# Optimization experiments

Measured on AMD Instinct MI355X. Metric: run time of the kernel, lower is better.

Reference implementation:

```python
import jax, jax.numpy as jnp
import numpy as np

NUM_HEADS = 4
WORD_DIM = 100
LEAKY_ALPHA = 0.3  # keras LeakyReLU default negative_slope


def setup_inputs() -> dict:
    key = jax.random.key(0)
    k1, k2, k3 = jax.random.split(key, 3)
    x = jax.random.normal(k1, (8, 30, 20, 40, WORD_DIM), dtype=jnp.float32)
    # keras 'random_normal' initializer: stddev 0.05
    w_att = jax.random.normal(k2, (NUM_HEADS, WORD_DIM), dtype=jnp.float32) * 0.05
    b_att = jax.random.normal(k3, (NUM_HEADS, WORD_DIM), dtype=jnp.float32) * 0.05
    return {"x": x, "w_att": w_att, "b_att": b_att}


def reference(x, w_att, b_att):
    # x: [B, T, E, W, D]; w_att, b_att: [H, D]
    B, T, E, W, D = x.shape
    H = w_att.shape[0]
    type_emb = x[..., 0, :]        # [B,T,E,D]
    words = x[..., 1:, :]          # [B,T,E,N,D], N = W-1
    # per-head hidden representation: leaky_relu(w*words + b)
    pre = words[..., None, :, :] * w_att[:, None, :] + b_att[:, None, :]  # [B,T,E,H,N,D]
    hidden = jnp.where(pre >= 0, pre, LEAKY_ALPHA * pre)
    # attention scores: dot(type_emb, hidden) over D
    scores = jnp.einsum('bted,btehnd->btehn', type_emb, hidden)  # [B,T,E,H,N]
    # original uses raw exp / sum (no max-subtraction) -- keep faithful
    att = jnp.exp(scores)
    att = att / jnp.sum(att, axis=-1, keepdims=True)
    out = jnp.einsum('btehn,btend->bthed'.replace('bthed', 'btehd'), att, words)  # [B,T,E,H,D]
    out = out.reshape(B, T, E, H * D)
    # all-zero events map to zero embeddings
    nonzero = jnp.any(x != 0, axis=(-1, -2), keepdims=False)  # [B,T,E]
    out = jnp.where(nonzero[..., None], out, 0.0)
    return out
```

## Files before the change

### kernel.cpp

```cpp
#include <hip/hip_runtime.h>
#include <math.h>
#include <stdint.h>

#define NHEAD 4
#define DD 100
#define NW 39
#define BLOCK 256

typedef __attribute__((address_space(3))) uint32_t lds_t;
typedef const __attribute__((address_space(1))) uint32_t glb_t;

__global__ __launch_bounds__(BLOCK, 8) void ts_enc(
    const float* __restrict__ x,
    const float* __restrict__ w_att,
    const float* __restrict__ b_att,
    float* __restrict__ out)
{
    __shared__ float tile[40 * DD];
    __shared__ float scp[4][NHEAD][40];
    __shared__ float att_T[40][NHEAD];

    const int tid  = threadIdx.x;
    const int wv   = __builtin_amdgcn_readfirstlane(tid >> 6);
    const int lane = tid & 63;
    const float* xsite = x + (size_t)blockIdx.x * (40 * DD);

    #pragma unroll
    for (int i = 0; i < 4; ++i) {
        const int cf = i * BLOCK + tid;
        if (cf < 1000) {
            glb_t* g = (glb_t*)(xsite + cf * 4);
            lds_t* l = (lds_t*)(tile + (i * BLOCK + wv * 64) * 4);
            __builtin_amdgcn_global_load_lds(g, l, 16, 0, 0);
        }
    }
    __syncthreads();

    const bool act  = lane < NW;
    const int  nrow = act ? lane : NW - 1;
    const float* wrow = tile + (1 + nrow) * DD;
    float acc[NHEAD] = {0.f, 0.f, 0.f, 0.f};

    for (int c = wv; c < 25; c += 4) {
        const float4 te4 = *(const float4*)(tile + c * 4);
        const float4 v4  = *(const float4*)(wrow + c * 4);
        const float a65x = 0.65f * te4.x, a35x = 0.35f * te4.x;
        const float a65y = 0.65f * te4.y, a35y = 0.35f * te4.y;
        const float a65z = 0.65f * te4.z, a35z = 0.35f * te4.z;
        const float a65w = 0.65f * te4.w, a35w = 0.35f * te4.w;
        #pragma unroll
        for (int h = 0; h < NHEAD; ++h) {
            const float4 w4 = *(const float4*)(w_att + h * DD + c * 4);
            const float4 b4 = *(const float4*)(b_att + h * DD + c * 4);
            float p0 = fmaf(v4.x, w4.x, b4.x);
            float p1 = fmaf(v4.y, w4.y, b4.y);
            float p2 = fmaf(v4.z, w4.z, b4.z);
            float p3 = fmaf(v4.w, w4.w, b4.w);
            float t  = fmaf(a65x, p0, fmaf(a35x, fabsf(p0), acc[h]));
            t        = fmaf(a65y, p1, fmaf(a35y, fabsf(p1), t));
            t        = fmaf(a65z, p2, fmaf(a35z, fabsf(p2), t));
            acc[h]   = fmaf(a65w, p3, fmaf(a35w, fabsf(p3), t));
        }
    }
    if (act) {
        scp[wv][0][lane] = acc[0];
        scp[wv][1][lane] = acc[1];
        scp[wv][2][lane] = acc[2];
        scp[wv][3][lane] = acc[3];
    }
    __syncthreads();

    float sc = -INFINITY;
    if (act) sc = (scp[0][wv][lane] + scp[1][wv][lane])
                + (scp[2][wv][lane] + scp[3][wv][lane]);
    float mx = sc;
    #pragma unroll
    for (int off = 32; off; off >>= 1) mx = fmaxf(mx, __shfl_xor(mx, off));
    float p = act ? __expf(sc - mx) : 0.f;
    float sm = p;
    #pragma unroll
    for (int off = 32; off; off >>= 1) sm += __shfl_xor(sm, off);
    if (act) att_T[lane][wv] = p / sm;
    __syncthreads();

    if (wv < 2) {
        const int h  = lane >> 4;
        const int dc = (wv << 4) + (lane & 15);
        if (dc < 25) {
            float4 ca = make_float4(0.f, 0.f, 0.f, 0.f);
            const float* wb = tile + DD + dc * 4;
            #pragma unroll
            for (int n = 0; n < NW; ++n) {
                const float attn = att_T[n][h];
                const float4 wd = *(const float4*)(wb + n * DD);
                ca.x = fmaf(attn, wd.x, ca.x);
                ca.y = fmaf(attn, wd.y, ca.y);
                ca.z = fmaf(attn, wd.z, ca.z);
                ca.w = fmaf(attn, wd.w, ca.w);
            }
            *(float4*)(out + (size_t)blockIdx.x * (NHEAD * DD) + h * DD + dc * 4) = ca;
        }
    }
}

extern "C" void kernel_launch(void* const* d_in, const int* in_sizes, int n_in,
                              void* d_out, int out_size, void* d_ws, size_t ws_size,
                              hipStream_t stream) {
    const float* x     = (const float*)d_in[0];
    const float* w_att = (const float*)d_in[1];
    const float* b_att = (const float*)d_in[2];
    float* out = (float*)d_out;

    const int sites = 8 * 30 * 20;
    ts_enc<<<sites, BLOCK, 0, stream>>>(x, w_att, b_att, out);
}
```

Baseline: 27.66 us.

## Split weighted-sum over word rows across two waves with LDS partial reduction

The output weighted sum previously had 50 of 128 lanes idle and each lane looped over all 39 word rows. Now two waves each handle half of the word rows, with every lane covering 2 columns for all 4 heads. Partial sums go to an aliased LDS buffer and are combined after an extra barrier. The type embedding is also read from global memory rather than LDS in the score loop. The cost is one extra __syncthreads, a second LDS round trip, and redundant global loads of the type row.

```diff
diff --git a/kernel.cpp b/kernel.cpp
--- a/kernel.cpp
+++ b/kernel.cpp
@@ -17,8 +17,11 @@
     float* __restrict__ out)
 {
     __shared__ float tile[40 * DD];
-    __shared__ float scp[4][NHEAD][40];
+    __shared__ float shbuf[800];
     __shared__ float att_T[40][NHEAD];
+
+    float (*scp)[NHEAD][40] = (float (*)[NHEAD][40])shbuf;
+    float (*P)[NHEAD][DD]   = (float (*)[NHEAD][DD])shbuf;
 
     const int tid  = threadIdx.x;
     const int wv   = __builtin_amdgcn_readfirstlane(tid >> 6);
@@ -42,7 +45,7 @@
     float acc[NHEAD] = {0.f, 0.f, 0.f, 0.f};
 
     for (int c = wv; c < 25; c += 4) {
-        const float4 te4 = *(const float4*)(tile + c * 4);
+        const float4 te4 = *(const float4*)(xsite + c * 4);
         const float4 v4  = *(const float4*)(wrow + c * 4);
         const float a65x = 0.65f * te4.x, a35x = 0.35f * te4.x;
         const float a65y = 0.65f * te4.y, a35y = 0.35f * te4.y;
@@ -84,22 +87,37 @@
     __syncthreads();
 
     if (wv < 2) {
-        const int h  = lane >> 4;
-        const int dc = (wv << 4) + (lane & 15);
-        if (dc < 25) {
-            float4 ca = make_float4(0.f, 0.f, 0.f, 0.f);
-            const float* wb = tile + DD + dc * 4;
-            #pragma unroll
-            for (int n = 0; n < NW; ++n) {
-                const float attn = att_T[n][h];
-                const float4 wd = *(const float4*)(wb + n * DD);
-                ca.x = fmaf(attn, wd.x, ca.x);
-                ca.y = fmaf(attn, wd.y, ca.y);
-                ca.z = fmaf(attn, wd.z, ca.z);
-                ca.w = fmaf(attn, wd.w, ca.w);
-            }
-            *(float4*)(out + (size_t)blockIdx.x * (NHEAD * DD) + h * DD + dc * 4) = ca;
+        const int l2 = lane < 50 ? lane : 49;
+        const float* wbase = tile + DD + l2 * 2;
+        float2 a0 = {0,0}, a1 = {0,0}, a2 = {0,0}, a3 = {0,0};
+        for (int n = wv; n < NW; n += 2) {
+            const float4 at = *(const float4*)&att_T[n][0];
+            const float2 wd = *(const float2*)(wbase + n * DD);
+            a0.x = fmaf(at.x, wd.x, a0.x); a0.y = fmaf(at.x, wd.y, a0.y);
+            a1.x = fmaf(at.y, wd.x, a1.x); a1.y = fmaf(at.y, wd.y, a1.y);
+            a2.x = fmaf(at.z, wd.x, a2.x); a2.y = fmaf(at.z, wd.y, a2.y);
+            a3.x = fmaf(at.w, wd.x, a3.x); a3.y = fmaf(at.w, wd.y, a3.y);
         }
+        if (lane < 50) {
+            *(float2*)&P[wv][0][lane * 2] = a0;
+            *(float2*)&P[wv][1][lane * 2] = a1;
+            *(float2*)&P[wv][2][lane * 2] = a2;
+            *(float2*)&P[wv][3][lane * 2] = a3;
+        }
+    }
+    __syncthreads();
+
+    if (tid < 100) {
+        const int h  = tid / 25;
+        const int c4 = tid - h * 25;
+        const float4 q0 = *(const float4*)&P[0][h][c4 * 4];
+        const float4 q1 = *(const float4*)&P[1][h][c4 * 4];
+        float4 r;
+        r.x = q0.x + q1.x;
+        r.y = q0.y + q1.y;
+        r.z = q0.z + q1.z;
+        r.w = q0.w + q1.w;
+        *(float4*)(out + (size_t)blockIdx.x * (NHEAD * DD) + h * DD + c4 * 4) = r;
     }
 }
 
```

After: 29.44 us. +6.5%, slower.
